# Optimization experiments

Measured on AMD Instinct MI355X. Metric: run time of the kernel, lower is better.

Reference implementation:

```python
import jax, jax.numpy as jnp
import numpy as np
from jax import lax

GEN_POLY = ("1111001", "1011011")  # rate 1/2, constraint length 7 (octal 171/133)


def build_trellis(gen_poly):
    """Feed-forward (non-recursive) convolutional trellis tables.

    State = shift-register contents, most-recent bit is the MSB of the state
    index. Returns int32 tables, each [ns, ni]:
      to_nodes[s, b]        : next state from state s with input bit b
      op_by_fromnode[s, b]  : emitted output-symbol index for (s, b)
      from_nodes[j, m]      : m-th predecessor state of state j
      ip_by_tonode[j, m]    : input bit taken on that predecessor transition
    """
    mu = len(gen_poly[0]) - 1
    ns, ni = 2 ** mu, 2
    g = np.array([[int(c) for c in p] for p in gen_poly])  # [conv_n, mu+1]
    to_nodes = np.zeros((ns, ni), np.int32)
    op_by_fromnode = np.zeros((ns, ni), np.int32)
    from_nodes = np.zeros((ns, ni), np.int32)
    ip_by_tonode = np.zeros((ns, ni), np.int32)
    fill = np.zeros(ns, np.int32)
    for s in range(ns):
        rbits = [(s >> (mu - 1 - j)) & 1 for j in range(mu)]
        for b in range(ni):
            w = np.array([b] + rbits)                 # full window [b, r0..r_{mu-1}]
            obits = (g @ w) % 2                        # output bits, MSB first
            o = int("".join(str(int(x)) for x in obits), 2)
            j = int("".join(str(x) for x in ([b] + rbits[:-1])), 2)
            to_nodes[s, b] = j
            op_by_fromnode[s, b] = o
            from_nodes[j, fill[j]] = s
            ip_by_tonode[j, fill[j]] = b
            fill[j] += 1
    return to_nodes, op_by_fromnode, from_nodes, ip_by_tonode


TO_NODES, OP_BY_FROM, FROM_NODES, IP_BY_TO = build_trellis(GEN_POLY)
CONV_N = len(GEN_POLY)
MU = len(GEN_POLY[0]) - 1
NS = 2 ** MU
NO = 2 ** CONV_N
# output-symbol bit patterns, MSB first, mapped to signs (1-2*bit)
_OP_BITS = np.array([[(o >> (CONV_N - 1 - j)) & 1 for j in range(CONV_N)]
                     for o in range(NO)], np.float32)
OP_SIGN = jnp.asarray(1.0 - 2.0 * _OP_BITS)  # [NO, CONV_N]
IP_SIGN = jnp.asarray([1.0, -1.0])           # sign of input bit b: 1-2b


def setup_inputs() -> dict:
    key = jax.random.key(0)
    k1, k2 = jax.random.split(key)
    B, n = 256, 4096
    T = n // CONV_N  # = k = 2048 info bits
    llr_ch = jax.random.normal(k1, (B, n), dtype=jnp.float32)
    llr_a = jax.random.normal(k2, (B, T), dtype=jnp.float32)
    return {"llr_ch": llr_ch, "llr_a": llr_a}


def _bcjr(llr_ch, llr_a):
    B, n = llr_ch.shape
    T = n // CONV_N
    # branch metrics: bm[t, b, o] = exp(0.5 * sum_j llr[b, t, j] * (1-2*opbit_j(o)))
    llr_r = llr_ch.reshape(B, T, CONV_N)
    bm = jnp.exp(0.5 * jnp.einsum('btj,oj->tbo', llr_r, OP_SIGN))  # [T, B, NO]
    llr_a_t = llr_a.T  # [T, B]

    def gamma_fn(bm_t, la_t):
        # a-priori factor exp(0.5*llr_a*(1-2b)) times channel branch metric
        ap = jnp.exp(0.5 * la_t[:, None, None] * IP_SIGN[None, None, :])  # [B,1,2]
        return ap * bm_t[:, OP_BY_FROM]  # [B, NS, 2]

    alpha0 = jnp.zeros((B, NS), jnp.float32).at[:, 0].set(1.0)

    def fwd(alpha_prev, inp):
        bm_t, la_t = inp
        gam = gamma_fn(bm_t, la_t)                        # [B, NS, 2] by from-state
        ag = gam * alpha_prev[:, :, None]                  # alpha_{t} * gamma_t
        agt = ag[:, FROM_NODES, IP_BY_TO]                  # regroup by to-state
        alpha = agt.sum(-1)
        alpha = alpha / alpha.sum(-1, keepdims=True)       # normalize (as in TF code)
        return alpha, alpha_prev                            # emit alpha BEFORE step t

    _, alphas = lax.scan(fwd, alpha0, (bm, llr_a_t))       # alphas[t] = alpha_t, [T,B,NS]

    beta_T = jnp.full((B, NS), 1.0 / NS, jnp.float32)      # non-terminated: uniform

    def bwd(beta_next, inp):
        bm_t, la_t, alpha_t = inp
        gam = gamma_fn(bm_t, la_t)                         # [B, NS, 2]
        bg = gam * beta_next[:, TO_NODES]                  # gamma * beta_{t+1}(to)
        beta = bg.sum(-1)
        beta = beta / beta.sum(-1, keepdims=True)
        joint = alpha_t[:, :, None] * bg                   # APP per (state, bit)
        llr_t = jnp.log(joint[..., 0].sum(-1)) - jnp.log(joint[..., 1].sum(-1))
        return beta, llr_t

    _, llrs_rev = lax.scan(bwd, beta_T, (bm[::-1], llr_a_t[::-1], alphas[::-1]))
    return llrs_rev[::-1].T  # [B, T] soft LLRs (hard_out=False)


def reference(llr_ch, llr_a):
    return _bcjr(llr_ch, llr_a)
```

## Files before the change

### kernel.cpp

```cpp
#include <hip/hip_runtime.h>

#define T_LEN 2048
#define NSTATE 64
#define NCHUNK 16
#define CH_S 128
#define HF 64
#define WARM 64
#define RK 16

template<int CTRL>
__device__ __forceinline__ float dpp_add(float v) {
    int r = __builtin_amdgcn_update_dpp(0, __float_as_int(v), CTRL, 0xF, 0xF, true);
    return v + __int_as_float(r);
}

__device__ __forceinline__ float dpp_mov_xor1(float v) {
    return __int_as_float(__builtin_amdgcn_update_dpp(0, __float_as_int(v), 0xB1, 0xF, 0xF, true));
}

__device__ __forceinline__ float dpp_sum_to63(float v) {
    v = dpp_add<0x111>(v);
    v = dpp_add<0x112>(v);
    v = dpp_add<0x114>(v);
    v = dpp_add<0x118>(v);
    v = dpp_add<0x142>(v);
    v = dpp_add<0x143>(v);
    return v;
}

__device__ __forceinline__ float wave_total(float v) {
    float s = dpp_sum_to63(v);
    return __int_as_float(__builtin_amdgcn_readlane(__float_as_int(s), 63));
}

__device__ __forceinline__ float pair_sum_xor1(float v) {
    int r = __builtin_amdgcn_update_dpp(0, __float_as_int(v), 0xB1, 0xF, 0xF, true);
    return v + __int_as_float(r);
}

__device__ __forceinline__ float bperm(int addrb, float v) {
    return __int_as_float(__builtin_amdgcn_ds_bpermute(addrb, __float_as_int(v)));
}

__device__ __forceinline__ unsigned short bf16_of(float f) {
    return (unsigned short)((__float_as_uint(f) + 0x8000u) >> 16);
}
__device__ __forceinline__ float bf16_ld(const unsigned short* p) {
    return __uint_as_float(((unsigned)*p) << 16);
}

__device__ __forceinline__ void llr_reduce_store(float na, float nb, int lane, float* dst) {
    na += __shfl_xor(na, 32, 64);
    nb += __shfl_xor(nb, 32, 64);
    float z = (lane >= 32) ? nb : na;
    z = dpp_add<0xB1>(z);
    z = dpp_add<0x4E>(z);
    z = dpp_add<0x124>(z);
    z = dpp_add<0x128>(z);
    z += __shfl_xor(z, 16, 64);
    float lg = __log2f(z);
    float d  = (lg - __shfl_xor(lg, 32, 64)) * 0.6931471805599453f;
    if (lane == 0) *dst = d;
}


template<int MODE>
__device__ __forceinline__ float fwd_group(float state,
                                           const float* __restrict__ chp,
                                           const float* __restrict__ lap,
                                           unsigned short* __restrict__ alds,
                                           const unsigned short* __restrict__ blds,
                                           float* __restrict__ outp,
                                           int g, int t0, int lane,
                                           float kE, float k0, float k1,
                                           int fselb)
{
    #pragma unroll
    for (int h = 0; h < 2; ++h) {
        const int gb = g + 8 * h;
        const float4* c4 = (const float4*)(chp + 2 * gb);
        const float4* a4 = (const float4*)(lap + gb);
        float4 cc[4], aa[2];
        #pragma unroll
        for (int i = 0; i < 4; ++i) cc[i] = c4[i];
        #pragma unroll
        for (int i = 0; i < 2; ++i) aa[i] = a4[i];
        float bv0[8], bv1[8];
        if (MODE == 2) {
            const unsigned short* bp = blds + (size_t)(gb - t0 - HF) * NSTATE + (lane >> 1);
            #pragma unroll
            for (int i = 0; i < 8; ++i) {
                bv0[i] = bf16_ld(bp + i * NSTATE);
                bv1[i] = bf16_ld(bp + i * NSTATE + 32);
            }
        }
        #pragma unroll
        for (int i = 0; i < 8; ++i) {
            float l0 = (i & 1) ? cc[i >> 1].z : cc[i >> 1].x;
            float l1 = (i & 1) ? cc[i >> 1].w : cc[i >> 1].y;
            float la = ((const float*)aa)[i];
            if (MODE == 1) alds[(gb + i - t0) * NSTATE + lane] = bf16_of(state);
            float x   = fmaf(la, kE, fmaf(l0, k0, l1 * k1));
            float g0v = exp2f(x);
            float g1v = __builtin_amdgcn_rcpf(g0v);
            float sg0 = state * g0v;
            float sg1 = state * g1v;
            if (MODE == 2)
                llr_reduce_store(sg0 * bv0[i], sg1 * bv1[i], lane, outp + gb + i);
            float s0 = pair_sum_xor1(sg0);
            float s1 = pair_sum_xor1(sg1);
            float v  = (lane & 1) ? s1 : s0;
            state = bperm(fselb, v);
        }
    }
    float s = wave_total(state);
    return state * __builtin_amdgcn_rcpf(s);
}

template<int MODE>
__device__ __forceinline__ float bwd_group(float state,
                                           const float* __restrict__ chp,
                                           const float* __restrict__ lap,
                                           const unsigned short* __restrict__ alds,
                                           unsigned short* __restrict__ blds,
                                           float* __restrict__ outp,
                                           int g, int t0, int lane,
                                           float kE, float k0, float k1,
                                           unsigned pmask, int bgb)
{
    const bool odd = (lane & 1);
    #pragma unroll
    for (int h = 1; h >= 0; --h) {
        const int gb = g + 8 * h;
        const float4* c4 = (const float4*)(chp + 2 * gb);
        const float4* a4 = (const float4*)(lap + gb);
        float4 cc[4], aa[2];
        #pragma unroll
        for (int i = 0; i < 4; ++i) cc[i] = c4[i];
        #pragma unroll
        for (int i = 0; i < 2; ++i) aa[i] = a4[i];
        float av[8];
        if (MODE == 2) {
            const unsigned short* ap = alds + (size_t)(gb - t0) * NSTATE + lane;
            #pragma unroll
            for (int i = 0; i < 8; ++i)
                av[i] = bf16_ld(ap + i * NSTATE);
        }
        #pragma unroll
        for (int i = 7; i >= 0; --i) {
            float l0 = (i & 1) ? cc[i >> 1].z : cc[i >> 1].x;
            float l1 = (i & 1) ? cc[i >> 1].w : cc[i >> 1].y;
            float la = ((const float*)aa)[i];
            if (MODE == 1) blds[(gb + i - t0 - HF) * NSTATE + lane] = bf16_of(state);
            float x  = fmaf(la, kE, fmaf(l0, k0, l1 * k1));
            float xg = __uint_as_float(__float_as_uint(x) ^ pmask);
            float ga  = exp2f(xg);
            float gb_ = __builtin_amdgcn_rcpf(ga);
            float a  = bperm(bgb, state);
            float bb = dpp_mov_xor1(a);
            float u0 = ga * a;
            float u1 = gb_ * bb;
            if (MODE == 2) {
                float ua = odd ? u1 : u0;
                float ub = odd ? u0 : u1;
                llr_reduce_store(av[i] * ua, av[i] * ub, lane, outp + gb + i);
            }
            state = u0 + u1;
        }
    }
    float s = wave_total(state);
    return state * __builtin_amdgcn_rcpf(s);
}

__global__ __launch_bounds__(128, 5)
void bcjr_fused_kernel(const float* __restrict__ llr_ch,
                       const float* __restrict__ llr_a,
                       float* __restrict__ out)
{
    __shared__ unsigned short alds[HF * NSTATE];
    __shared__ unsigned short blds[HF * NSTATE];

    const int lane  = threadIdx.x & 63;
    const int role  = threadIdx.x >> 6;
    const int unit  = blockIdx.x;
    const int chunk = unit & (NCHUNK - 1);
    const int b     = unit >> 4;

    const float c0 = 1.0f - 2.0f * (float)(__popc(lane & 57) & 1);
    const float c1 = 1.0f - 2.0f * (float)(__popc(lane & 27) & 1);
    const float kE = 0.5f * 1.442695040888963f;
    const float k0 = kE * c0, k1 = kE * c1;

    const float* chp = llr_ch + (size_t)b * (2 * T_LEN);
    const float* lap = llr_a  + (size_t)b * T_LEN;
    float* outp = out + (size_t)b * T_LEN;
    const int t0 = chunk * CH_S;

    if (role == 0) {
        const int fselb = (2 * (lane & 31) + (lane >> 5)) << 2;
        float state = (chunk == 0) ? ((lane == 0) ? 1.0f : 0.0f) : (1.0f / 64.0f);
        const int ts = (chunk == 0) ? t0 : t0 - WARM;
        for (int g = ts; g < t0; g += RK)
            state = fwd_group<0>(state, chp, lap, alds, blds, outp, g, t0, lane, kE, k0, k1, fselb);
        for (int g = t0; g < t0 + HF; g += RK)
            state = fwd_group<1>(state, chp, lap, alds, blds, outp, g, t0, lane, kE, k0, k1, fselb);
        __syncthreads();
        for (int g = t0 + HF; g < t0 + CH_S; g += RK)
            state = fwd_group<2>(state, chp, lap, alds, blds, outp, g, t0, lane, kE, k0, k1, fselb);
    } else {
        const unsigned pmask = (unsigned)(lane & 1) << 31;
        const int bgb = ((lane >> 1) + ((lane & 1) << 5)) << 2;
        float state = 1.0f / 64.0f;
        const int te = (chunk == NCHUNK - 1) ? (t0 + CH_S) : (t0 + CH_S + WARM);
        for (int g = te - RK; g >= t0 + CH_S; g -= RK)
            state = bwd_group<0>(state, chp, lap, alds, blds, outp, g, t0, lane, kE, k0, k1, pmask, bgb);
        for (int g = t0 + CH_S - RK; g >= t0 + HF; g -= RK)
            state = bwd_group<1>(state, chp, lap, alds, blds, outp, g, t0, lane, kE, k0, k1, pmask, bgb);
        __syncthreads();
        for (int g = t0 + HF - RK; g >= t0; g -= RK)
            state = bwd_group<2>(state, chp, lap, alds, blds, outp, g, t0, lane, kE, k0, k1, pmask, bgb);
    }
}

extern "C" void kernel_launch(void* const* d_in, const int* in_sizes, int n_in,
                              void* d_out, int out_size, void* d_ws, size_t ws_size,
                              hipStream_t stream) {
    const float* llr_ch = (const float*)d_in[0];
    const float* llr_a  = (const float*)d_in[1];
    float* out = (float*)d_out;

    int B = in_sizes[0] / (2 * T_LEN);
    (void)d_ws; (void)ws_size;

    int n_units = B * NCHUNK;
    hipLaunchKernelGGL(bcjr_fused_kernel, dim3(n_units), dim3(128), 0, stream,
                       llr_ch, llr_a, out);
}
```

Measured before the change: 131.6 us.

## Transpose bf16 LDS history to state-major rows with packed 128-bit accesses

Stores the alpha/beta bf16 history in LDS as state-major rows (padded to 36 words), so each lane packs 8 timesteps into one 128-bit store and reads them back with one 128-bit load instead of eight 16-bit accesses. The LLR reduction changes from a shuffle/DPP mix to two full-wave DPP prefix sums with the result taken in lane 63, which drops the cross-half shuffles but adds an extra log per step. The launch-bounds occupancy hint drops from 5 to 4, likely to give room for the extra registers needed for packing.

New measurement: 129.0 us. -2.0%, faster.

```diff
diff --git a/kernel.cpp b/kernel.cpp
--- a/kernel.cpp
+++ b/kernel.cpp
@@ -7,6 +7,7 @@
 #define HF 64
 #define WARM 64
 #define RK 16
+#define ROWQ 36
 
 template<int CTRL>
 __device__ __forceinline__ float dpp_add(float v) {
@@ -42,25 +43,12 @@
     return __int_as_float(__builtin_amdgcn_ds_bpermute(addrb, __float_as_int(v)));
 }
 
-__device__ __forceinline__ unsigned short bf16_of(float f) {
-    return (unsigned short)((__float_as_uint(f) + 0x8000u) >> 16);
-}
-__device__ __forceinline__ float bf16_ld(const unsigned short* p) {
-    return __uint_as_float(((unsigned)*p) << 16);
-}
-
-__device__ __forceinline__ void llr_reduce_store(float na, float nb, int lane, float* dst) {
-    na += __shfl_xor(na, 32, 64);
-    nb += __shfl_xor(nb, 32, 64);
-    float z = (lane >= 32) ? nb : na;
-    z = dpp_add<0xB1>(z);
-    z = dpp_add<0x4E>(z);
-    z = dpp_add<0x124>(z);
-    z = dpp_add<0x128>(z);
-    z += __shfl_xor(z, 16, 64);
-    float lg = __log2f(z);
-    float d  = (lg - __shfl_xor(lg, 32, 64)) * 0.6931471805599453f;
-    if (lane == 0) *dst = d;
+__device__ __forceinline__ unsigned bf16_of(float f) {
+    return (__float_as_uint(f) + 0x8000u) >> 16;
+}
+template<int HI>
+__device__ __forceinline__ float bf16_half(unsigned w) {
+    return __uint_as_float(HI ? (w & 0xffff0000u) : (w << 16));
 }
 
 
@@ -68,8 +56,8 @@
 __device__ __forceinline__ float fwd_group(float state,
                                            const float* __restrict__ chp,
                                            const float* __restrict__ lap,
-                                           unsigned short* __restrict__ alds,
-                                           const unsigned short* __restrict__ blds,
+                                           unsigned* __restrict__ alds,
+                                           const unsigned* __restrict__ blds,
                                            float* __restrict__ outp,
                                            int g, int t0, int lane,
                                            float kE, float k0, float k1,
@@ -85,33 +73,45 @@
         for (int i = 0; i < 4; ++i) cc[i] = c4[i];
         #pragma unroll
         for (int i = 0; i < 2; ++i) aa[i] = a4[i];
-        float bv0[8], bv1[8];
+        uint4 bw0, bw1;
         if (MODE == 2) {
-            const unsigned short* bp = blds + (size_t)(gb - t0 - HF) * NSTATE + (lane >> 1);
-            #pragma unroll
-            for (int i = 0; i < 8; ++i) {
-                bv0[i] = bf16_ld(bp + i * NSTATE);
-                bv1[i] = bf16_ld(bp + i * NSTATE + 32);
-            }
+            const int off = (gb - t0 - HF) >> 1;
+            bw0 = *(const uint4*)(blds + (lane >> 1) * ROWQ + off);
+            bw1 = *(const uint4*)(blds + (32 + (lane >> 1)) * ROWQ + off);
         }
+        unsigned pk[4];
         #pragma unroll
         for (int i = 0; i < 8; ++i) {
             float l0 = (i & 1) ? cc[i >> 1].z : cc[i >> 1].x;
             float l1 = (i & 1) ? cc[i >> 1].w : cc[i >> 1].y;
             float la = ((const float*)aa)[i];
-            if (MODE == 1) alds[(gb + i - t0) * NSTATE + lane] = bf16_of(state);
+            if (MODE == 1) {
+                unsigned hs = bf16_of(state);
+                if (i & 1) pk[i >> 1] |= hs << 16; else pk[i >> 1] = hs;
+            }
             float x   = fmaf(la, kE, fmaf(l0, k0, l1 * k1));
             float g0v = exp2f(x);
             float g1v = __builtin_amdgcn_rcpf(g0v);
             float sg0 = state * g0v;
             float sg1 = state * g1v;
-            if (MODE == 2)
-                llr_reduce_store(sg0 * bv0[i], sg1 * bv1[i], lane, outp + gb + i);
+            if (MODE == 2) {
+                unsigned w0 = (&bw0.x)[i >> 1];
+                unsigned w1 = (&bw1.x)[i >> 1];
+                float b0v = (i & 1) ? bf16_half<1>(w0) : bf16_half<0>(w0);
+                float b1v = (i & 1) ? bf16_half<1>(w1) : bf16_half<0>(w1);
+                float na = dpp_sum_to63(sg0 * b0v);
+                float nb = dpp_sum_to63(sg1 * b1v);
+                if (lane == 63)
+                    outp[gb + i] = (__log2f(na) - __log2f(nb)) * 0.6931471805599453f;
+            }
             float s0 = pair_sum_xor1(sg0);
             float s1 = pair_sum_xor1(sg1);
             float v  = (lane & 1) ? s1 : s0;
             state = bperm(fselb, v);
         }
+        if (MODE == 1)
+            *(uint4*)(alds + lane * ROWQ + ((gb - t0) >> 1)) =
+                make_uint4(pk[0], pk[1], pk[2], pk[3]);
     }
     float s = wave_total(state);
     return state * __builtin_amdgcn_rcpf(s);
@@ -121,8 +121,8 @@
 __device__ __forceinline__ float bwd_group(float state,
                                            const float* __restrict__ chp,
                                            const float* __restrict__ lap,
-                                           const unsigned short* __restrict__ alds,
-                                           unsigned short* __restrict__ blds,
+                                           const unsigned* __restrict__ alds,
+                                           unsigned* __restrict__ blds,
                                            float* __restrict__ outp,
                                            int g, int t0, int lane,
                                            float kE, float k0, float k1,
@@ -139,19 +139,19 @@
         for (int i = 0; i < 4; ++i) cc[i] = c4[i];
         #pragma unroll
         for (int i = 0; i < 2; ++i) aa[i] = a4[i];
-        float av[8];
-        if (MODE == 2) {
-            const unsigned short* ap = alds + (size_t)(gb - t0) * NSTATE + lane;
-            #pragma unroll
-            for (int i = 0; i < 8; ++i)
-                av[i] = bf16_ld(ap + i * NSTATE);
-        }
+        uint4 aw;
+        if (MODE == 2)
+            aw = *(const uint4*)(alds + lane * ROWQ + ((gb - t0) >> 1));
+        unsigned pk[4];
         #pragma unroll
         for (int i = 7; i >= 0; --i) {
             float l0 = (i & 1) ? cc[i >> 1].z : cc[i >> 1].x;
             float l1 = (i & 1) ? cc[i >> 1].w : cc[i >> 1].y;
             float la = ((const float*)aa)[i];
-            if (MODE == 1) blds[(gb + i - t0 - HF) * NSTATE + lane] = bf16_of(state);
+            if (MODE == 1) {
+                unsigned hs = bf16_of(state);
+                if (i & 1) pk[i >> 1] = hs << 16; else pk[i >> 1] |= hs;
+            }
             float x  = fmaf(la, kE, fmaf(l0, k0, l1 * k1));
             float xg = __uint_as_float(__float_as_uint(x) ^ pmask);
             float ga  = exp2f(xg);
@@ -161,24 +161,32 @@
             float u0 = ga * a;
             float u1 = gb_ * bb;
             if (MODE == 2) {
+                unsigned w = (&aw.x)[i >> 1];
+                float av = (i & 1) ? bf16_half<1>(w) : bf16_half<0>(w);
                 float ua = odd ? u1 : u0;
                 float ub = odd ? u0 : u1;
-                llr_reduce_store(av[i] * ua, av[i] * ub, lane, outp + gb + i);
+                float na = dpp_sum_to63(av * ua);
+                float nb = dpp_sum_to63(av * ub);
+                if (lane == 63)
+                    outp[gb + i] = (__log2f(na) - __log2f(nb)) * 0.6931471805599453f;
             }
             state = u0 + u1;
         }
+        if (MODE == 1)
+            *(uint4*)(blds + lane * ROWQ + ((gb - t0 - HF) >> 1)) =
+                make_uint4(pk[0], pk[1], pk[2], pk[3]);
     }
     float s = wave_total(state);
     return state * __builtin_amdgcn_rcpf(s);
 }
 
-__global__ __launch_bounds__(128, 5)
+__global__ __launch_bounds__(128, 4)
 void bcjr_fused_kernel(const float* __restrict__ llr_ch,
                        const float* __restrict__ llr_a,
                        float* __restrict__ out)
 {
-    __shared__ unsigned short alds[HF * NSTATE];
-    __shared__ unsigned short blds[HF * NSTATE];
+    __shared__ __align__(16) unsigned alds[NSTATE * ROWQ];
+    __shared__ __align__(16) unsigned blds[NSTATE * ROWQ];
 
     const int lane  = threadIdx.x & 63;
     const int role  = threadIdx.x >> 6;
```
